# Optimization experiments

Hardware: AMD Instinct MI355X
Metric: run time of the kernel (lower is better)

Reference implementation:

```python
import jax, jax.numpy as jnp
import numpy as np

N_NODES = 10000
N_FEATS = 128
BSZ = 32
D = 100000


def setup_inputs() -> dict:
    key = jax.random.key(0)
    k_vals, k_idx = jax.random.split(key)
    flat_inputs = jax.random.normal(k_vals, (BSZ, D), dtype=jnp.float32)
    # Sample D UNIQUE (node, feat) slots per batch row so the scatter has no
    # duplicate destinations (torch duplicate writes are nondeterministic).
    n_slots = N_NODES * N_FEATS
    keys = jax.random.split(k_idx, BSZ)
    flat_pos = jax.vmap(lambda k: jax.random.permutation(k, n_slots)[:D])(keys)  # [BSZ, D]
    node_ids = (flat_pos // N_FEATS).astype(jnp.int64)
    feat_ids = (flat_pos % N_FEATS).astype(jnp.int64)
    return {"flat_inputs": flat_inputs, "node_ids": node_ids, "feat_ids": feat_ids}


def reference(flat_inputs, node_ids, feat_ids):
    bsz, d = flat_inputs.shape
    # Linearize (batch, node, feat) -> single flat index; one fused scatter.
    batch_ids = jnp.arange(bsz, dtype=node_ids.dtype)[:, None]  # [bsz, 1] broadcasts over D
    lin = (batch_ids * N_NODES + node_ids) * N_FEATS + feat_ids  # [bsz, D]
    obs_mat = jnp.zeros((bsz * N_NODES * N_FEATS,), dtype=flat_inputs.dtype)
    obs_mat = obs_mat.at[lin.reshape(-1)].set(flat_inputs.reshape(-1), unique_indices=True)
    return obs_mat.reshape(bsz, N_NODES, N_FEATS)
```

## Files before the change

kernel.cpp:

```cpp
#include <hip/hip_runtime.h>
#include <stdint.h>

#define N_NODES 10000
#define N_FEATS 128
#define BSZ 32
#define D_ELEMS 100000

#define OUT_ELEMS (BSZ * N_NODES * N_FEATS)
#define N_ITEMS   (BSZ * D_ELEMS)
#define N_GROUPS  (N_ITEMS / 4)

#define NBUCKET 512
#define CHUNK   (OUT_ELEMS / NBUCKET)
#define CAP     8064
#define SUBF    8000
#define NSUB    (CHUNK / SUBF)

#define BIN_GPB   1024
#define BIN_IPB   (BIN_GPB * 4)
#define BIN_NBLK  ((N_GROUPS + BIN_GPB - 1) / BIN_GPB)

typedef float f32x4 __attribute__((ext_vector_type(4)));
typedef int   i32x4 __attribute__((ext_vector_type(4)));

__global__ __launch_bounds__(512) void bin_kernel(
    const f32x4* __restrict__ vals,
    const i32x4* __restrict__ nodes,
    const i32x4* __restrict__ feats,
    uint64_t* __restrict__ pairs,
    uint32_t* __restrict__ gcount) {
  __shared__ uint32_t hist[NBUCKET];
  __shared__ uint32_t excl[NBUCKET];
  __shared__ uint32_t base_s[NBUCKET];
  __shared__ uint32_t wpart[8];
  __shared__ uint32_t tot_s;
  __shared__ alignas(16) uint64_t sp[BIN_IPB];
  const int tid = threadIdx.x;
  hist[tid] = 0;
  __syncthreads();

  uint32_t lin[8]; float val[8]; uint32_t rnk[8];
  const int gbase = blockIdx.x * BIN_GPB;
#pragma unroll
  for (int q = 0; q < 2; ++q) {
    int g = gbase + q * 512 + tid;
    bool a = (g < N_GROUPS);
    int gg = a ? g : 0;
    f32x4 v = vals[gg];
    i32x4 n = nodes[gg];
    i32x4 f = feats[gg];
    uint32_t rowbase = (uint32_t)((gg * 4) / D_ELEMS) * (uint32_t)(N_NODES * N_FEATS);
    lin[q*4+0] = a ? rowbase + (uint32_t)n.x * N_FEATS + (uint32_t)f.x : 0xFFFFFFFFu;
    lin[q*4+1] = a ? rowbase + (uint32_t)n.y * N_FEATS + (uint32_t)f.y : 0xFFFFFFFFu;
    lin[q*4+2] = a ? rowbase + (uint32_t)n.z * N_FEATS + (uint32_t)f.z : 0xFFFFFFFFu;
    lin[q*4+3] = a ? rowbase + (uint32_t)n.w * N_FEATS + (uint32_t)f.w : 0xFFFFFFFFu;
    val[q*4+0] = v.x; val[q*4+1] = v.y; val[q*4+2] = v.z; val[q*4+3] = v.w;
  }

#pragma unroll
  for (int i = 0; i < 8; ++i)
    if (lin[i] != 0xFFFFFFFFu)
      rnk[i] = atomicAdd(&hist[lin[i] / CHUNK], 1u);
  __syncthreads();

  uint32_t h = hist[tid];
  uint32_t v = h;
#pragma unroll
  for (int s = 1; s < 64; s <<= 1) {
    uint32_t u = __shfl_up(v, s, 64);
    if ((tid & 63) >= s) v += u;
  }
  if ((tid & 63) == 63) wpart[tid >> 6] = v;
  __syncthreads();
  if (tid < 64) {
    uint32_t p = (tid < 8) ? wpart[tid] : 0u;
#pragma unroll
    for (int s = 1; s < 8; s <<= 1) {
      uint32_t u = __shfl_up(p, s, 64);
      if (tid >= s) p += u;
    }
    if (tid < 8) wpart[tid] = p;
  }
  __syncthreads();
  uint32_t woff = (tid >= 64) ? wpart[(tid >> 6) - 1] : 0u;
  uint32_t incl = v + woff;
  excl[tid] = incl - h;
  base_s[tid] = h ? atomicAdd(&gcount[tid], h) : 0u;
  if (tid == 511) tot_s = incl;
  __syncthreads();

#pragma unroll
  for (int i = 0; i < 8; ++i) {
    if (lin[i] != 0xFFFFFFFFu) {
      uint32_t b = lin[i] / CHUNK;
      sp[excl[b] + rnk[i]] =
          ((uint64_t)__float_as_uint(val[i]) << 32) | (uint64_t)lin[i];
    }
  }
  __syncthreads();

  const uint32_t tot = tot_s;
  for (uint32_t i = tid; i < tot; i += 512u) {
    uint64_t p = sp[i];
    uint32_t l = (uint32_t)p;
    uint32_t b = l / CHUNK;
    uint32_t dst = base_s[b] + (i - excl[b]);
    if (dst < CAP) pairs[(size_t)b * CAP + dst] = p;
  }
}

__global__ __launch_bounds__(1024) void expand_kernel(
    const uint64_t* __restrict__ pairs,
    const uint32_t* __restrict__ gcount,
    float* __restrict__ out) {
  __shared__ alignas(16) float chunk[2 * SUBF];
  const int b = blockIdx.x;
  const int tid = threadIdx.x;
  uint32_t cnt = gcount[b];
  if (cnt > CAP) cnt = CAP;

  uint32_t ml[8];
  float    mv[8];
  const uint64_t* bp = pairs + (size_t)b * CAP;
  const uint32_t cbase = (uint32_t)(b * CHUNK);
#pragma unroll
  for (int i = 0; i < 8; ++i) {
    uint32_t idx = (uint32_t)tid + (uint32_t)i * 1024u;
    uint64_t p = (idx < cnt) ? bp[idx] : ~0ull;
    ml[i] = (uint32_t)p - cbase;
    mv[i] = __uint_as_float((uint32_t)(p >> 32));
  }

  f32x4* c4 = (f32x4*)chunk;
  const f32x4 z = {0.f, 0.f, 0.f, 0.f};
#pragma unroll
  for (int j = 0; j < 4; ++j) {
    int idx = tid + j * 1024;
    if (idx < (2 * SUBF) / 4) c4[idx] = z;
  }
  __syncthreads();

#pragma unroll
  for (int i = 0; i < 8; ++i)
    if (ml[i] < SUBF) chunk[ml[i]] = mv[i];
  __syncthreads();

  const size_t outbase = (size_t)b * CHUNK;
  for (int p = 0; p < NSUB; ++p) {
    if (p + 1 < NSUB) {
      uint32_t lo = (uint32_t)((p + 1) * SUBF);
      float* dsth = chunk + ((p + 1) & 1) * SUBF;
#pragma unroll
      for (int i = 0; i < 8; ++i) {
        uint32_t loc = ml[i] - lo;
        if (loc < SUBF) dsth[loc] = mv[i];
      }
    }
    f32x4* src = (f32x4*)(chunk + (p & 1) * SUBF);
    f32x4* o4  = (f32x4*)(out + outbase + (size_t)p * SUBF);
#pragma unroll
    for (int j = 0; j < 2; ++j) {
      int idx = tid + j * 1024;
      if (idx < SUBF / 4) {
        f32x4 w = src[idx];
        src[idx] = z;
        o4[idx] = w;
      }
    }
    __syncthreads();
  }
}

__global__ __launch_bounds__(256) void scatter4_kernel(
    const f32x4* __restrict__ vals,
    const i32x4* __restrict__ node_ids,
    const i32x4* __restrict__ feat_ids,
    float* __restrict__ out) {
  int t = blockIdx.x * blockDim.x + threadIdx.x;
  if (t >= N_GROUPS) return;
  int b = (t * 4) / D_ELEMS;
  f32x4 v = vals[t];
  i32x4 n = node_ids[t];
  i32x4 f = feat_ids[t];
  size_t base = (size_t)b * N_NODES * N_FEATS;
  out[base + (size_t)n.x * N_FEATS + (size_t)f.x] = v.x;
  out[base + (size_t)n.y * N_FEATS + (size_t)f.y] = v.y;
  out[base + (size_t)n.z * N_FEATS + (size_t)f.z] = v.z;
  out[base + (size_t)n.w * N_FEATS + (size_t)f.w] = v.w;
}

extern "C" void kernel_launch(void* const* d_in, const int* in_sizes, int n_in,
                              void* d_out, int out_size, void* d_ws, size_t ws_size,
                              hipStream_t stream) {
  const float* vals     = (const float*)d_in[0];
  const int*   node_ids = (const int*)d_in[1];
  const int*   feat_ids = (const int*)d_in[2];
  float* out = (float*)d_out;

  const size_t pairs_bytes = (size_t)NBUCKET * CAP * sizeof(uint64_t);
  const size_t need = pairs_bytes + NBUCKET * sizeof(uint32_t);

  if (ws_size >= need) {
    uint64_t* pairs  = (uint64_t*)d_ws;
    uint32_t* gcount = (uint32_t*)((char*)d_ws + pairs_bytes);
    hipMemsetAsync(gcount, 0, NBUCKET * sizeof(uint32_t), stream);
    bin_kernel<<<BIN_NBLK, 512, 0, stream>>>(
        (const f32x4*)vals, (const i32x4*)node_ids, (const i32x4*)feat_ids,
        pairs, gcount);
    expand_kernel<<<NBUCKET, 1024, 0, stream>>>(pairs, gcount, out);
  } else {
    hipMemsetAsync(out, 0, (size_t)out_size * sizeof(float), stream);
    const int grid = (N_GROUPS + 255) / 256;
    scatter4_kernel<<<grid, 256, 0, stream>>>(
        (const f32x4*)vals, (const i32x4*)node_ids, (const i32x4*)feat_ids, out);
  }
}
```

Measured before the change: 49.10 us.

## Double bucket count and store compact 16-bit offsets with separate values

Doubles the number of output buckets to 1024, which halves each bucket's chunk to 40000 elements so an in-bucket offset fits in 16 bits. Intermediate pairs are now stored as separate uint16 offset and float value arrays instead of packed 64-bit words, cutting workspace traffic between the binning and expand kernels from 8 to 6 bytes per item. The change also gives the expand kernel twice as many blocks to spread across CUs. In exchange there are more histogram buckets and global atomics per bin block, and less headroom in CAP (4416 against a mean of about 3125 items per bucket).

```diff
diff --git a/kernel.cpp b/kernel.cpp
--- a/kernel.cpp
+++ b/kernel.cpp
@@ -10,9 +10,9 @@
 #define N_ITEMS   (BSZ * D_ELEMS)
 #define N_GROUPS  (N_ITEMS / 4)
 
-#define NBUCKET 512
+#define NBUCKET 1024
 #define CHUNK   (OUT_ELEMS / NBUCKET)
-#define CAP     8064
+#define CAP     4416
 #define SUBF    8000
 #define NSUB    (CHUNK / SUBF)
 
@@ -27,16 +27,19 @@
     const f32x4* __restrict__ vals,
     const i32x4* __restrict__ nodes,
     const i32x4* __restrict__ feats,
-    uint64_t* __restrict__ pairs,
+    uint16_t* __restrict__ offs,
+    float*    __restrict__ pvals,
     uint32_t* __restrict__ gcount) {
   __shared__ uint32_t hist[NBUCKET];
   __shared__ uint32_t excl[NBUCKET];
   __shared__ uint32_t base_s[NBUCKET];
   __shared__ uint32_t wpart[8];
   __shared__ uint32_t tot_s;
-  __shared__ alignas(16) uint64_t sp[BIN_IPB];
+  __shared__ uint32_t sl[BIN_IPB];
+  __shared__ float    sv[BIN_IPB];
   const int tid = threadIdx.x;
   hist[tid] = 0;
+  hist[tid + 512] = 0;
   __syncthreads();
 
   uint32_t lin[8]; float val[8]; uint32_t rnk[8];
@@ -63,8 +66,9 @@
       rnk[i] = atomicAdd(&hist[lin[i] / CHUNK], 1u);
   __syncthreads();
 
-  uint32_t h = hist[tid];
-  uint32_t v = h;
+  uint32_t h0 = hist[2*tid], h1 = hist[2*tid + 1];
+  uint32_t hp = h0 + h1;
+  uint32_t v = hp;
 #pragma unroll
   for (int s = 1; s < 64; s <<= 1) {
     uint32_t u = __shfl_up(v, s, 64);
@@ -83,34 +87,42 @@
   }
   __syncthreads();
   uint32_t woff = (tid >= 64) ? wpart[(tid >> 6) - 1] : 0u;
-  uint32_t incl = v + woff;
-  excl[tid] = incl - h;
-  base_s[tid] = h ? atomicAdd(&gcount[tid], h) : 0u;
-  if (tid == 511) tot_s = incl;
+  uint32_t e = (v + woff) - hp;
+  excl[2*tid]     = e;
+  excl[2*tid + 1] = e + h0;
+  base_s[2*tid]     = h0 ? atomicAdd(&gcount[2*tid], h0) : 0u;
+  base_s[2*tid + 1] = h1 ? atomicAdd(&gcount[2*tid + 1], h1) : 0u;
+  if (tid == 511) tot_s = e + hp;
   __syncthreads();
 
 #pragma unroll
   for (int i = 0; i < 8; ++i) {
     if (lin[i] != 0xFFFFFFFFu) {
       uint32_t b = lin[i] / CHUNK;
-      sp[excl[b] + rnk[i]] =
-          ((uint64_t)__float_as_uint(val[i]) << 32) | (uint64_t)lin[i];
+      uint32_t slot = excl[b] + rnk[i];
+      sl[slot] = lin[i];
+      sv[slot] = val[i];
     }
   }
   __syncthreads();
 
   const uint32_t tot = tot_s;
   for (uint32_t i = tid; i < tot; i += 512u) {
-    uint64_t p = sp[i];
-    uint32_t l = (uint32_t)p;
+    uint32_t l = sl[i];
+    float    w = sv[i];
     uint32_t b = l / CHUNK;
     uint32_t dst = base_s[b] + (i - excl[b]);
-    if (dst < CAP) pairs[(size_t)b * CAP + dst] = p;
+    if (dst < CAP) {
+      size_t o = (size_t)b * CAP + dst;
+      offs[o]  = (uint16_t)(l - b * CHUNK);
+      pvals[o] = w;
+    }
   }
 }
 
 __global__ __launch_bounds__(1024) void expand_kernel(
-    const uint64_t* __restrict__ pairs,
+    const uint16_t* __restrict__ offs,
+    const float*    __restrict__ pvals,
     const uint32_t* __restrict__ gcount,
     float* __restrict__ out) {
   __shared__ alignas(16) float chunk[2 * SUBF];
@@ -119,16 +131,15 @@
   uint32_t cnt = gcount[b];
   if (cnt > CAP) cnt = CAP;
 
-  uint32_t ml[8];
-  float    mv[8];
-  const uint64_t* bp = pairs + (size_t)b * CAP;
-  const uint32_t cbase = (uint32_t)(b * CHUNK);
-#pragma unroll
-  for (int i = 0; i < 8; ++i) {
+  uint32_t ml[5]; float mv[5];
+  const uint16_t* bo = offs  + (size_t)b * CAP;
+  const float*    bv = pvals + (size_t)b * CAP;
+#pragma unroll
+  for (int i = 0; i < 5; ++i) {
     uint32_t idx = (uint32_t)tid + (uint32_t)i * 1024u;
-    uint64_t p = (idx < cnt) ? bp[idx] : ~0ull;
-    ml[i] = (uint32_t)p - cbase;
-    mv[i] = __uint_as_float((uint32_t)(p >> 32));
+    bool a = (idx < cnt);
+    ml[i] = a ? (uint32_t)bo[idx] : 0xFFFFFFFFu;
+    mv[i] = a ? bv[idx] : 0.f;
   }
 
   f32x4* c4 = (f32x4*)chunk;
@@ -141,7 +152,7 @@
   __syncthreads();
 
 #pragma unroll
-  for (int i = 0; i < 8; ++i)
+  for (int i = 0; i < 5; ++i)
     if (ml[i] < SUBF) chunk[ml[i]] = mv[i];
   __syncthreads();
 
@@ -151,7 +162,7 @@
       uint32_t lo = (uint32_t)((p + 1) * SUBF);
       float* dsth = chunk + ((p + 1) & 1) * SUBF;
 #pragma unroll
-      for (int i = 0; i < 8; ++i) {
+      for (int i = 0; i < 5; ++i) {
         uint32_t loc = ml[i] - lo;
         if (loc < SUBF) dsth[loc] = mv[i];
       }
@@ -197,17 +208,19 @@
   const int*   feat_ids = (const int*)d_in[2];
   float* out = (float*)d_out;
 
-  const size_t pairs_bytes = (size_t)NBUCKET * CAP * sizeof(uint64_t);
-  const size_t need = pairs_bytes + NBUCKET * sizeof(uint32_t);
+  const size_t offs_bytes = (size_t)NBUCKET * CAP * sizeof(uint16_t);
+  const size_t pval_bytes = (size_t)NBUCKET * CAP * sizeof(float);
+  const size_t need = offs_bytes + pval_bytes + NBUCKET * sizeof(uint32_t);
 
   if (ws_size >= need) {
-    uint64_t* pairs  = (uint64_t*)d_ws;
-    uint32_t* gcount = (uint32_t*)((char*)d_ws + pairs_bytes);
+    uint16_t* offs   = (uint16_t*)d_ws;
+    float*    pvals  = (float*)((char*)d_ws + offs_bytes);
+    uint32_t* gcount = (uint32_t*)((char*)d_ws + offs_bytes + pval_bytes);
     hipMemsetAsync(gcount, 0, NBUCKET * sizeof(uint32_t), stream);
     bin_kernel<<<BIN_NBLK, 512, 0, stream>>>(
         (const f32x4*)vals, (const i32x4*)node_ids, (const i32x4*)feat_ids,
-        pairs, gcount);
-    expand_kernel<<<NBUCKET, 1024, 0, stream>>>(pairs, gcount, out);
+        offs, pvals, gcount);
+    expand_kernel<<<NBUCKET, 1024, 0, stream>>>(offs, pvals, gcount, out);
   } else {
     hipMemsetAsync(out, 0, (size_t)out_size * sizeof(float), stream);
     const int grid = (N_GROUPS + 255) / 256;
```

Result: slower. 50.45 us (+2.8%).

## Split binning and expansion into two halves to overlap stages in a mixed kernel

Applied to the files above, without the earlier changes.

Input groups are split into two stages by batch half, each binned into its own half of the buckets. A mixed kernel expands the first half of the buckets while binning the second half, so the write-bound expand work overlaps the atomic-heavy binning. Expansion now uses 512-thread blocks that each handle 16 items per thread instead of 1024 threads handling 8. The cost is an extra kernel launch, manually carved shared memory that sizes every mixed-kernel block for the larger expand footprint, and a correctness dependence on the first batch half covering exactly the first half of the buckets.

```diff
diff --git a/kernel.cpp b/kernel.cpp
--- a/kernel.cpp
+++ b/kernel.cpp
@@ -16,40 +16,47 @@
 #define SUBF    8000
 #define NSUB    (CHUNK / SUBF)
 
-#define BIN_GPB   1024
-#define BIN_IPB   (BIN_GPB * 4)
-#define BIN_NBLK  ((N_GROUPS + BIN_GPB - 1) / BIN_GPB)
+#define STAGE_GROUPS (N_GROUPS / 2)
+#define SBUCKET (NBUCKET / 2)
+#define BIN_GPB  1024
+#define BIN_NBLK ((STAGE_GROUPS + BIN_GPB - 1) / BIN_GPB)
+
+#define BIN_SMEM 35872
+#define EXP_SMEM 64000
 
 typedef float f32x4 __attribute__((ext_vector_type(4)));
 typedef int   i32x4 __attribute__((ext_vector_type(4)));
 
-__global__ __launch_bounds__(512) void bin_kernel(
+__device__ __forceinline__ void bin_device(
+    int s, int bblk, int tid,
     const f32x4* __restrict__ vals,
     const i32x4* __restrict__ nodes,
     const i32x4* __restrict__ feats,
     uint64_t* __restrict__ pairs,
-    uint32_t* __restrict__ gcount) {
-  __shared__ uint32_t hist[NBUCKET];
-  __shared__ uint32_t excl[NBUCKET];
-  __shared__ uint32_t base_s[NBUCKET];
-  __shared__ uint32_t wpart[8];
-  __shared__ uint32_t tot_s;
-  __shared__ alignas(16) uint64_t sp[BIN_IPB];
-  const int tid = threadIdx.x;
-  hist[tid] = 0;
+    uint32_t* __restrict__ gcount,
+    uint8_t* smem) {
+  uint64_t* sp     = (uint64_t*)smem;
+  uint32_t* hist   = (uint32_t*)(smem + 32768);
+  uint32_t* excl   = (uint32_t*)(smem + 33792);
+  uint32_t* base_s = (uint32_t*)(smem + 34816);
+  uint32_t* wpart  = (uint32_t*)(smem + 35840);
+  uint32_t* tot_p  = (uint32_t*)(smem + 35856);
+
+  if (tid < SBUCKET) hist[tid] = 0;
   __syncthreads();
 
   uint32_t lin[8]; float val[8]; uint32_t rnk[8];
-  const int gbase = blockIdx.x * BIN_GPB;
+  const int lbase = bblk * BIN_GPB;
+  const uint32_t bb0 = (uint32_t)s * SBUCKET;
 #pragma unroll
   for (int q = 0; q < 2; ++q) {
-    int g = gbase + q * 512 + tid;
-    bool a = (g < N_GROUPS);
-    int gg = a ? g : 0;
-    f32x4 v = vals[gg];
-    i32x4 n = nodes[gg];
-    i32x4 f = feats[gg];
-    uint32_t rowbase = (uint32_t)((gg * 4) / D_ELEMS) * (uint32_t)(N_NODES * N_FEATS);
+    int lg = lbase + q * 512 + tid;
+    bool a = (lg < STAGE_GROUPS);
+    int g = a ? (s * STAGE_GROUPS + lg) : 0;
+    f32x4 v = vals[g];
+    i32x4 n = nodes[g];
+    i32x4 f = feats[g];
+    uint32_t rowbase = (uint32_t)((g * 4) / D_ELEMS) * (uint32_t)(N_NODES * N_FEATS);
     lin[q*4+0] = a ? rowbase + (uint32_t)n.x * N_FEATS + (uint32_t)f.x : 0xFFFFFFFFu;
     lin[q*4+1] = a ? rowbase + (uint32_t)n.y * N_FEATS + (uint32_t)f.y : 0xFFFFFFFFu;
     lin[q*4+2] = a ? rowbase + (uint32_t)n.z * N_FEATS + (uint32_t)f.z : 0xFFFFFFFFu;
@@ -60,72 +67,77 @@
 #pragma unroll
   for (int i = 0; i < 8; ++i)
     if (lin[i] != 0xFFFFFFFFu)
-      rnk[i] = atomicAdd(&hist[lin[i] / CHUNK], 1u);
-  __syncthreads();
-
-  uint32_t h = hist[tid];
-  uint32_t v = h;
-#pragma unroll
-  for (int s = 1; s < 64; s <<= 1) {
-    uint32_t u = __shfl_up(v, s, 64);
-    if ((tid & 63) >= s) v += u;
-  }
-  if ((tid & 63) == 63) wpart[tid >> 6] = v;
+      rnk[i] = atomicAdd(&hist[lin[i] / CHUNK - bb0], 1u);
+  __syncthreads();
+
+  uint32_t h = 0, v = 0;
+  if (tid < SBUCKET) {
+    h = hist[tid];
+    v = h;
+#pragma unroll
+    for (int st = 1; st < 64; st <<= 1) {
+      uint32_t u = __shfl_up(v, st, 64);
+      if ((tid & 63) >= st) v += u;
+    }
+    if ((tid & 63) == 63) wpart[tid >> 6] = v;
+  }
   __syncthreads();
   if (tid < 64) {
-    uint32_t p = (tid < 8) ? wpart[tid] : 0u;
-#pragma unroll
-    for (int s = 1; s < 8; s <<= 1) {
-      uint32_t u = __shfl_up(p, s, 64);
-      if (tid >= s) p += u;
-    }
-    if (tid < 8) wpart[tid] = p;
-  }
-  __syncthreads();
-  uint32_t woff = (tid >= 64) ? wpart[(tid >> 6) - 1] : 0u;
-  uint32_t incl = v + woff;
-  excl[tid] = incl - h;
-  base_s[tid] = h ? atomicAdd(&gcount[tid], h) : 0u;
-  if (tid == 511) tot_s = incl;
+    uint32_t p = (tid < 4) ? wpart[tid] : 0u;
+#pragma unroll
+    for (int st = 1; st < 4; st <<= 1) {
+      uint32_t u = __shfl_up(p, st, 64);
+      if (tid >= st) p += u;
+    }
+    if (tid < 4) wpart[tid] = p;
+  }
+  __syncthreads();
+  if (tid < SBUCKET) {
+    uint32_t woff = (tid >= 64) ? wpart[(tid >> 6) - 1] : 0u;
+    uint32_t incl = v + woff;
+    excl[tid] = incl - h;
+    base_s[tid] = h ? atomicAdd(&gcount[bb0 + tid], h) : 0u;
+    if (tid == SBUCKET - 1) *tot_p = incl;
+  }
   __syncthreads();
 
 #pragma unroll
   for (int i = 0; i < 8; ++i) {
     if (lin[i] != 0xFFFFFFFFu) {
-      uint32_t b = lin[i] / CHUNK;
-      sp[excl[b] + rnk[i]] =
+      uint32_t bl = lin[i] / CHUNK - bb0;
+      sp[excl[bl] + rnk[i]] =
           ((uint64_t)__float_as_uint(val[i]) << 32) | (uint64_t)lin[i];
     }
   }
   __syncthreads();
 
-  const uint32_t tot = tot_s;
+  const uint32_t tot = *tot_p;
   for (uint32_t i = tid; i < tot; i += 512u) {
     uint64_t p = sp[i];
     uint32_t l = (uint32_t)p;
-    uint32_t b = l / CHUNK;
-    uint32_t dst = base_s[b] + (i - excl[b]);
-    if (dst < CAP) pairs[(size_t)b * CAP + dst] = p;
-  }
-}
-
-__global__ __launch_bounds__(1024) void expand_kernel(
+    uint32_t gb = l / CHUNK;
+    uint32_t bl = gb - bb0;
+    uint32_t dst = base_s[bl] + (i - excl[bl]);
+    if (dst < CAP) pairs[(size_t)gb * CAP + dst] = p;
+  }
+}
+
+__device__ __forceinline__ void expand_device(
+    int eb, int tid,
     const uint64_t* __restrict__ pairs,
     const uint32_t* __restrict__ gcount,
-    float* __restrict__ out) {
-  __shared__ alignas(16) float chunk[2 * SUBF];
-  const int b = blockIdx.x;
-  const int tid = threadIdx.x;
-  uint32_t cnt = gcount[b];
+    float* __restrict__ out,
+    uint8_t* smem) {
+  float* chunk = (float*)smem;
+  uint32_t cnt = gcount[eb];
   if (cnt > CAP) cnt = CAP;
 
-  uint32_t ml[8];
-  float    mv[8];
-  const uint64_t* bp = pairs + (size_t)b * CAP;
-  const uint32_t cbase = (uint32_t)(b * CHUNK);
-#pragma unroll
-  for (int i = 0; i < 8; ++i) {
-    uint32_t idx = (uint32_t)tid + (uint32_t)i * 1024u;
+  uint32_t ml[16]; float mv[16];
+  const uint64_t* bp = pairs + (size_t)eb * CAP;
+  const uint32_t cbase = (uint32_t)eb * (uint32_t)CHUNK;
+#pragma unroll
+  for (int i = 0; i < 16; ++i) {
+    uint32_t idx = (uint32_t)tid + (uint32_t)i * 512u;
     uint64_t p = (idx < cnt) ? bp[idx] : ~0ull;
     ml[i] = (uint32_t)p - cbase;
     mv[i] = __uint_as_float((uint32_t)(p >> 32));
@@ -134,24 +146,24 @@
   f32x4* c4 = (f32x4*)chunk;
   const f32x4 z = {0.f, 0.f, 0.f, 0.f};
 #pragma unroll
-  for (int j = 0; j < 4; ++j) {
-    int idx = tid + j * 1024;
+  for (int j = 0; j < 8; ++j) {
+    int idx = tid + j * 512;
     if (idx < (2 * SUBF) / 4) c4[idx] = z;
   }
   __syncthreads();
 
 #pragma unroll
-  for (int i = 0; i < 8; ++i)
+  for (int i = 0; i < 16; ++i)
     if (ml[i] < SUBF) chunk[ml[i]] = mv[i];
   __syncthreads();
 
-  const size_t outbase = (size_t)b * CHUNK;
+  const size_t outbase = (size_t)eb * CHUNK;
   for (int p = 0; p < NSUB; ++p) {
     if (p + 1 < NSUB) {
       uint32_t lo = (uint32_t)((p + 1) * SUBF);
       float* dsth = chunk + ((p + 1) & 1) * SUBF;
 #pragma unroll
-      for (int i = 0; i < 8; ++i) {
+      for (int i = 0; i < 16; ++i) {
         uint32_t loc = ml[i] - lo;
         if (loc < SUBF) dsth[loc] = mv[i];
       }
@@ -159,8 +171,8 @@
     f32x4* src = (f32x4*)(chunk + (p & 1) * SUBF);
     f32x4* o4  = (f32x4*)(out + outbase + (size_t)p * SUBF);
 #pragma unroll
-    for (int j = 0; j < 2; ++j) {
-      int idx = tid + j * 1024;
+    for (int j = 0; j < 4; ++j) {
+      int idx = tid + j * 512;
       if (idx < SUBF / 4) {
         f32x4 w = src[idx];
         src[idx] = z;
@@ -169,6 +181,33 @@
     }
     __syncthreads();
   }
+}
+
+__global__ __launch_bounds__(512) void binA_kernel(
+    const f32x4* __restrict__ vals, const i32x4* __restrict__ nodes,
+    const i32x4* __restrict__ feats, uint64_t* __restrict__ pairs,
+    uint32_t* __restrict__ gcount) {
+  __shared__ alignas(16) uint8_t smem[BIN_SMEM];
+  bin_device(0, blockIdx.x, threadIdx.x, vals, nodes, feats, pairs, gcount, smem);
+}
+
+__global__ __launch_bounds__(512) void mixed_kernel(
+    const f32x4* __restrict__ vals, const i32x4* __restrict__ nodes,
+    const i32x4* __restrict__ feats, uint64_t* __restrict__ pairs,
+    uint32_t* __restrict__ gcount, float* __restrict__ out) {
+  __shared__ alignas(16) uint8_t smem[EXP_SMEM];
+  if (blockIdx.x < SBUCKET)
+    expand_device(blockIdx.x, threadIdx.x, pairs, gcount, out, smem);
+  else
+    bin_device(1, blockIdx.x - SBUCKET, threadIdx.x, vals, nodes, feats,
+               pairs, gcount, smem);
+}
+
+__global__ __launch_bounds__(512) void expandB_kernel(
+    const uint64_t* __restrict__ pairs, const uint32_t* __restrict__ gcount,
+    float* __restrict__ out) {
+  __shared__ alignas(16) uint8_t smem[EXP_SMEM];
+  expand_device(SBUCKET + blockIdx.x, threadIdx.x, pairs, gcount, out, smem);
 }
 
 __global__ __launch_bounds__(256) void scatter4_kernel(
@@ -192,9 +231,9 @@
 extern "C" void kernel_launch(void* const* d_in, const int* in_sizes, int n_in,
                               void* d_out, int out_size, void* d_ws, size_t ws_size,
                               hipStream_t stream) {
-  const float* vals     = (const float*)d_in[0];
-  const int*   node_ids = (const int*)d_in[1];
-  const int*   feat_ids = (const int*)d_in[2];
+  const f32x4* vals  = (const f32x4*)d_in[0];
+  const i32x4* nodes = (const i32x4*)d_in[1];
+  const i32x4* feats = (const i32x4*)d_in[2];
   float* out = (float*)d_out;
 
   const size_t pairs_bytes = (size_t)NBUCKET * CAP * sizeof(uint64_t);
@@ -204,14 +243,13 @@
     uint64_t* pairs  = (uint64_t*)d_ws;
     uint32_t* gcount = (uint32_t*)((char*)d_ws + pairs_bytes);
     hipMemsetAsync(gcount, 0, NBUCKET * sizeof(uint32_t), stream);
-    bin_kernel<<<BIN_NBLK, 512, 0, stream>>>(
-        (const f32x4*)vals, (const i32x4*)node_ids, (const i32x4*)feat_ids,
-        pairs, gcount);
-    expand_kernel<<<NBUCKET, 1024, 0, stream>>>(pairs, gcount, out);
+    binA_kernel<<<BIN_NBLK, 512, 0, stream>>>(vals, nodes, feats, pairs, gcount);
+    mixed_kernel<<<SBUCKET + BIN_NBLK, 512, 0, stream>>>(vals, nodes, feats,
+                                                         pairs, gcount, out);
+    expandB_kernel<<<SBUCKET, 512, 0, stream>>>(pairs, gcount, out);
   } else {
     hipMemsetAsync(out, 0, (size_t)out_size * sizeof(float), stream);
     const int grid = (N_GROUPS + 255) / 256;
-    scatter4_kernel<<<grid, 256, 0, stream>>>(
-        (const f32x4*)vals, (const i32x4*)node_ids, (const i32x4*)feat_ids, out);
-  }
-}
+    scatter4_kernel<<<grid, 256, 0, stream>>>(vals, nodes, feats, out);
+  }
+}
```

Measured after the change: 57.15 us. +16.4%, slower.
